# Optimization experiments

Measured on AMD Instinct MI355X. Metric: run time of the kernel, lower is better.

The kernel has to match this reference:

```python
import math
import jax, jax.numpy as jnp
import numpy as np

B, A, M, NC = 32, 8400, 32, 80
TOP_K, ALPHA, BETA, EPS = 13, 1.0, 6.0, 1e-9
IMG = 640.0


def _ciou(b1, b2, eps=1e-7):
    # b1, b2 broadcastable [..., 4]; CIoU as in compute_iou (box1=gt, box2=pred)
    b1x1, b1y1, b1x2, b1y2 = b1[..., 0], b1[..., 1], b1[..., 2], b1[..., 3]
    b2x1, b2y1, b2x2, b2y2 = b2[..., 0], b2[..., 1], b2[..., 2], b2[..., 3]
    w1, h1 = b1x2 - b1x1, b1y2 - b1y1 + eps
    w2, h2 = b2x2 - b2x1, b2y2 - b2y1 + eps
    inter = (jnp.minimum(b1x2, b2x2) - jnp.maximum(b1x1, b2x1)).clip(0) * \
            (jnp.minimum(b1y2, b2y2) - jnp.maximum(b1y1, b2y1)).clip(0)
    union = w1 * h1 + w2 * h2 - inter + eps
    iou = inter / union
    cw = jnp.maximum(b1x2, b2x2) - jnp.minimum(b1x1, b2x1)
    ch = jnp.maximum(b1y2, b2y2) - jnp.minimum(b1y1, b2y1)
    c2 = cw ** 2 + ch ** 2 + eps
    rho2 = ((b2x1 + b2x2 - b1x1 - b1x2) ** 2 + (b2y1 + b2y2 - b1y1 - b1y2) ** 2) / 4.0
    v = (4.0 / math.pi ** 2) * (jnp.arctan(w2 / h2) - jnp.arctan(w1 / h1)) ** 2
    alpha = jax.lax.stop_gradient(v / (v - iou + (1.0 + eps)))
    return iou - (rho2 / c2 + v * alpha)


def setup_inputs() -> dict:
    key = jax.random.key(0)
    ks = jax.random.split(key, 8)
    pd_scores = jax.random.uniform(ks[0], (B, A, NC), jnp.float32)
    anc_points = jax.random.uniform(ks[1], (A, 2), jnp.float32) * IMG
    # predicted boxes around anchor points (valid x1<x2, y1<y2)
    off = jax.random.uniform(ks[2], (B, A, 4), jnp.float32) * 80.0 + 2.0
    pd_bboxes = jnp.concatenate([anc_points[None] - off[..., :2],
                                 anc_points[None] + off[..., 2:]], -1)
    # GT boxes: random centers and sizes, clipped to image
    c = jax.random.uniform(ks[3], (B, M, 2), jnp.float32) * IMG
    wh = jax.random.uniform(ks[4], (B, M, 2), jnp.float32) * 180.0 + 20.0
    gt_bboxes = jnp.concatenate([(c - wh / 2).clip(0, IMG), (c + wh / 2).clip(0, IMG)], -1)
    gt_labels = jax.random.randint(ks[5], (B, M, 1), 0, NC, jnp.int64)
    n_valid = jax.random.randint(ks[6], (B,), 1, M + 1)
    mask_gt = (jnp.arange(M)[None, :] < n_valid[:, None]).astype(jnp.float32)[..., None]
    return {"pd_scores": pd_scores, "pd_bboxes": pd_bboxes, "anc_points": anc_points,
            "gt_labels": gt_labels, "gt_bboxes": gt_bboxes, "mask_gt": mask_gt}


def reference(pd_scores, pd_bboxes, anc_points, gt_labels, gt_bboxes, mask_gt):
    b, a, nc = pd_scores.shape
    m = gt_bboxes.shape[1]
    dtype = pd_scores.dtype

    # anchors-inside-GT mask: [B,M,A]
    lt = gt_bboxes[:, :, None, :2]          # [B,M,1,2]
    rb = gt_bboxes[:, :, None, 2:]
    deltas = jnp.concatenate([anc_points[None, None] - lt,
                              rb - anc_points[None, None]], -1)  # [B,M,A,4]
    mask_in_gts = deltas.min(-1) > EPS
    mg = mask_gt[..., 0] > 0                 # [B,M] bool
    gt_mask = mask_in_gts & mg[:, :, None]

    # per-GT class score gather: pd_scores[b, :, gt_labels[b,m]] -> [B,M,A]
    labels = gt_labels[..., 0]               # [B,M]
    idx = jnp.broadcast_to(labels[:, :, None, None], (b, m, a, 1))
    gathered = jnp.take_along_axis(jnp.broadcast_to(pd_scores[:, None], (b, m, a, nc)), idx, axis=3)[..., 0]
    bbox_scores = jnp.where(gt_mask, gathered, 0.0)

    # CIoU overlaps (dense, masked) [B,M,A]
    iou = _ciou(gt_bboxes[:, :, None, :], pd_bboxes[:, None, :, :])
    overlaps = jnp.where(gt_mask, jnp.maximum(iou, 0.0), 0.0)

    align_metric = bbox_scores ** ALPHA * overlaps ** BETA

    # top-k selection with duplicate suppression (faithful to scatter_add loop)
    _, tk_idx = jax.lax.top_k(align_metric, TOP_K)      # [B,M,K]
    tk_mask = jnp.broadcast_to(mg[:, :, None], tk_idx.shape)
    tk_idx = jnp.where(tk_mask, tk_idx, 0)
    bi = jnp.arange(b)[:, None, None]
    mi = jnp.arange(m)[None, :, None]
    counts = jnp.zeros((b, m, a), jnp.int32).at[bi, mi, tk_idx].add(1)
    mask_top_k = jnp.where(counts > 1, 0, counts).astype(dtype)

    mask_pos = mask_top_k * mask_in_gts.astype(dtype) * mg[:, :, None].astype(dtype)
    fg_mask = mask_pos.sum(1)                            # [B,A]

    # resolve anchors assigned to multiple GTs (no-op when none; matches torch branch)
    mask_multi = fg_mask[:, None, :] > 1                 # [B,M,A] (broadcast)
    max_idx = overlaps.argmax(1)                         # [B,A]
    is_max = (jnp.arange(m)[None, :, None] == max_idx[:, None, :]).astype(dtype)
    mask_pos = jnp.where(mask_multi, is_max, mask_pos)
    fg_mask = mask_pos.sum(1)

    target_gt_idx = mask_pos.argmax(1)                   # [B,A]
    target_labels = jnp.maximum(jnp.take_along_axis(labels, target_gt_idx, axis=1), 0)
    target_bboxes = jnp.take_along_axis(
        gt_bboxes, jnp.broadcast_to(target_gt_idx[..., None], (b, a, 4)), axis=1)

    target_scores = jax.nn.one_hot(target_labels, NC, dtype=dtype)
    target_scores = jnp.where((fg_mask > 0)[..., None], target_scores, 0.0)

    am = align_metric * mask_pos
    pos_am = am.max(-1, keepdims=True)                   # [B,M,1]
    pos_ov = (overlaps * mask_pos).max(-1, keepdims=True)
    norm = (am * pos_ov / (pos_am + EPS)).max(1)[..., None]  # [B,A,1]
    target_scores = target_scores * norm

    return target_bboxes, target_scores, fg_mask > 0
```

## Files before the change

kernel.cpp:

```cpp
#include <hip/hip_runtime.h>
#include <math.h>

#define BB 32
#define AA 8400
#define MM 32
#define NCC 80
#define TOPK 13
#define CAP 1024

__device__ __forceinline__ void wave_argmax(float& v, int& i) {
    #pragma unroll
    for (int off = 32; off > 0; off >>= 1) {
        float ov = __shfl_xor(v, off, 64);
        int oi = __shfl_xor(i, off, 64);
        if (ov > v || (ov == v && oi < i)) { v = ov; i = oi; }
    }
}

__global__ __launch_bounds__(256) void k12_topk(
        const float* __restrict__ pd_scores, const float* __restrict__ pd_bboxes,
        const float* __restrict__ anc, const int* __restrict__ gt_labels,
        const float* __restrict__ gt_bboxes, const float* __restrict__ mask_gt,
        unsigned char* __restrict__ mpos, float* __restrict__ pos_am, float* __restrict__ pos_ov) {
    __shared__ float lval[CAP];
    __shared__ int   lidx[CAP];
    __shared__ unsigned int bmask[(AA + 31) / 32];
    __shared__ float wv[4];
    __shared__ int   wi[4];
    __shared__ int   cnt, pcnt;
    const float eps = 1e-7f;
    int bm = blockIdx.x;
    int b = bm >> 5;
    int tid = threadIdx.x;
    long row = (long)bm * AA;
    if (tid == 0) { pos_am[bm] = 0.f; pos_ov[bm] = 0.f; cnt = 0; pcnt = 0; }
    unsigned int* mp4 = reinterpret_cast<unsigned int*>(mpos + row);
    for (int i = tid; i < AA / 4; i += 256) mp4[i] = 0u;
    if (!(mask_gt[bm] > 0.f)) return;

    for (int i = tid; i < (AA + 31) / 32; i += 256) bmask[i] = 0u;
    float4 g = reinterpret_cast<const float4*>(gt_bboxes)[bm];
    __syncthreads();

    #pragma unroll
    for (int j = 0; j < 33; j++) {
        int i = tid + (j << 8);
        if (i < AA) {
            float2 an = reinterpret_cast<const float2*>(anc)[i];
            float dmin = fminf(fminf(an.x - g.x, an.y - g.y), fminf(g.z - an.x, g.w - an.y));
            if (dmin > 1e-9f) {
                int s = atomicAdd(&cnt, 1);
                if (s < CAP) lidx[s] = i;
            }
        }
    }
    __syncthreads();
    int n_c = min(cnt, CAP);

    float w1 = g.z - g.x, h1 = g.w - g.y + eps;
    float atg = atanf(w1 / h1);
    float w1h1 = w1 * h1;
    float sgx = g.x + g.z, sgy = g.y + g.w;
    int lab = gt_labels[bm];
    const float4* pbb = reinterpret_cast<const float4*>(pd_bboxes) + (long)b * AA;
    const float* scp = pd_scores + (long)b * AA * NCC + lab;
    for (int s = tid; s < n_c; s += 256) {
        int i = lidx[s];
        float4 pb = pbb[i];
        float w2 = pb.z - pb.x, h2 = pb.w - pb.y + eps;
        float iw = fmaxf(fminf(g.z, pb.z) - fmaxf(g.x, pb.x), 0.f);
        float ih = fmaxf(fminf(g.w, pb.w) - fmaxf(g.y, pb.y), 0.f);
        float inter = iw * ih;
        float uni = w1h1 + w2 * h2 - inter + eps;
        float iou = inter / uni;
        float cw = fmaxf(g.z, pb.z) - fminf(g.x, pb.x);
        float ch = fmaxf(g.w, pb.w) - fminf(g.y, pb.y);
        float c2 = cw * cw + ch * ch + eps;
        float dx = pb.x + pb.z - sgx, dy = pb.y + pb.w - sgy;
        float rho2 = (dx * dx + dy * dy) * 0.25f;
        float dv = atanf(w2 / h2) - atg;
        float v = 0.4052847345693511f * dv * dv;
        float alpha = v / (v - iou + (1.0f + eps));
        float cv = iou - (rho2 / c2 + v * alpha);
        float ov = fmaxf(cv, 0.f);
        float sc = scp[(long)i * NCC];
        float o2 = ov * ov;
        float val = sc * o2 * o2 * o2;
        if (val > 0.f) {
            lval[s] = val;
            atomicAdd(&pcnt, 1);
            atomicOr(&bmask[i >> 5], 1u << (i & 31));
        } else {
            lval[s] = -1.f;
        }
    }
    for (int s = n_c + tid; s < CAP; s += 256) { lval[s] = -1.f; lidx[s] = AA; }
    __syncthreads();
    int p = pcnt;

    if (p >= TOPK) {
        float v0 = lval[tid], v1 = lval[tid + 256], v2 = lval[tid + 512], v3 = lval[tid + 768];
        int   i0 = lidx[tid], i1 = lidx[tid + 256], i2 = lidx[tid + 512], i3 = lidx[tid + 768];
        for (int k = 0; k < TOPK; k++) {
            float bv = v0; int bi = i0;
            if (v1 > bv || (v1 == bv && i1 < bi)) { bv = v1; bi = i1; }
            if (v2 > bv || (v2 == bv && i2 < bi)) { bv = v2; bi = i2; }
            if (v3 > bv || (v3 == bv && i3 < bi)) { bv = v3; bi = i3; }
            wave_argmax(bv, bi);
            if ((tid & 63) == 0) { wv[tid >> 6] = bv; wi[tid >> 6] = bi; }
            __syncthreads();
            float gv = wv[0]; int gi = wi[0];
            #pragma unroll
            for (int w = 1; w < 4; w++) {
                float ov = wv[w]; int oi = wi[w];
                if (ov > gv || (ov == gv && oi < gi)) { gv = ov; gi = oi; }
            }
            if (tid == 0) mpos[row + gi] = 1;
            if (i0 == gi) v0 = -1.f;
            if (i1 == gi) v1 = -1.f;
            if (i2 == gi) v2 = -1.f;
            if (i3 == gi) v3 = -1.f;
            __syncthreads();
        }
    } else {
        for (int s = tid; s < n_c; s += 256)
            if (lval[s] > 0.f) mpos[row + lidx[s]] = 1;
        if (tid == 0) {
            int rem = TOPK - p;
            for (int i = 0; rem > 0 && i < AA; i++) {
                if (!((bmask[i >> 5] >> (i & 31)) & 1u)) {
                    rem--;
                    float ax = anc[i * 2], ay = anc[i * 2 + 1];
                    float dmin = fminf(fminf(ax - g.x, ay - g.y), fminf(g.z - ax, g.w - ay));
                    if (dmin > 1e-9f) mpos[row + i] = 1;
                }
            }
        }
    }
}

__global__ __launch_bounds__(256) void k3_resolve(
        const float* __restrict__ pd_scores, const float* __restrict__ pd_bboxes,
        const float* __restrict__ anc, const int* __restrict__ gt_labels,
        const float* __restrict__ gt_bboxes, const float* __restrict__ mask_gt,
        const unsigned char* __restrict__ mpos,
        float* __restrict__ pos_am, float* __restrict__ pos_ov,
        float* __restrict__ out_bbox, float* __restrict__ out_fg,
        float* __restrict__ amval, int* __restrict__ packed) {
    __shared__ float sg[MM][8];
    __shared__ int slab[MM];
    __shared__ int smg[MM];
    const float eps = 1e-7f;
    int b = blockIdx.y;
    int tid = threadIdx.x;
    if (tid < MM) {
        int gm = b * MM + tid;
        float4 g = reinterpret_cast<const float4*>(gt_bboxes)[gm];
        float w1 = g.z - g.x, h1 = g.w - g.y + eps;
        sg[tid][0] = g.x; sg[tid][1] = g.y; sg[tid][2] = g.z; sg[tid][3] = g.w;
        sg[tid][4] = w1 * h1;
        sg[tid][5] = atanf(w1 / h1);
        sg[tid][6] = g.x + g.z;
        sg[tid][7] = g.y + g.w;
        int lb = gt_labels[gm]; if (lb < 0) lb = 0;
        slab[tid] = lb;
        smg[tid] = mask_gt[gm] > 0.f ? 1 : 0;
    }
    __syncthreads();
    int a = blockIdx.x * 256 + tid;
    if (a >= AA) return;
    float ax = anc[a * 2], ay = anc[a * 2 + 1];
    float4 pb = reinterpret_cast<const float4*>(pd_bboxes)[b * AA + a];
    float w2 = pb.z - pb.x, h2 = pb.w - pb.y + eps;
    float atp = atanf(w2 / h2);
    float w2h2 = w2 * h2;
    float spx = pb.x + pb.z, spy = pb.y + pb.w;
    long mbase = (long)b * MM * AA + a;

    int fg = 0, firstm = -1, bestm = 0;
    float bestov = -1.f, ovsel = 0.f;
    for (int m = 0; m < MM; m++) {
        float gx1 = sg[m][0], gy1 = sg[m][1], gx2 = sg[m][2], gy2 = sg[m][3];
        float dmin = fminf(fminf(ax - gx1, ay - gy1), fminf(gx2 - ax, gy2 - ay));
        float ov = 0.f;
        if ((dmin > 1e-9f) && smg[m]) {
            float iw = fmaxf(fminf(gx2, pb.z) - fmaxf(gx1, pb.x), 0.f);
            float ih = fmaxf(fminf(gy2, pb.w) - fmaxf(gy1, pb.y), 0.f);
            float inter = iw * ih;
            float uni = sg[m][4] + w2h2 - inter + eps;
            float iou = inter / uni;
            float cw = fmaxf(gx2, pb.z) - fminf(gx1, pb.x);
            float ch = fmaxf(gy2, pb.w) - fminf(gy1, pb.y);
            float c2 = cw * cw + ch * ch + eps;
            float dx = spx - sg[m][6], dy = spy - sg[m][7];
            float rho2 = (dx * dx + dy * dy) * 0.25f;
            float dv = atp - sg[m][5];
            float v = 0.4052847345693511f * dv * dv;
            float alpha = v / (v - iou + (1.0f + eps));
            float cv = iou - (rho2 / c2 + v * alpha);
            ov = fmaxf(cv, 0.f);
        }
        if (ov > bestov) { bestov = ov; bestm = m; }
        if (mpos[mbase + (long)m * AA]) {
            if (fg == 0) { firstm = m; ovsel = ov; }
            fg++;
        }
    }
    int tg; bool fgo; float ovt;
    if (fg > 1) { tg = bestm; fgo = true;  ovt = bestov; }
    else        { tg = (fg == 1) ? firstm : 0; fgo = (fg == 1); ovt = (fg == 1) ? ovsel : 0.f; }

    int g = b * AA + a;
    float4 gb; gb.x = sg[tg][0]; gb.y = sg[tg][1]; gb.z = sg[tg][2]; gb.w = sg[tg][3];
    reinterpret_cast<float4*>(out_bbox)[g] = gb;
    out_fg[g] = fgo ? 1.f : 0.f;
    float amv = 0.f;
    if (fgo) {
        float sc = pd_scores[((long)b * AA + a) * NCC + slab[tg]];
        float o2 = ovt * ovt;
        amv = sc * o2 * o2 * o2;
        atomicMax((int*)&pos_am[b * MM + tg], __float_as_int(amv));
        atomicMax((int*)&pos_ov[b * MM + tg], __float_as_int(ovt));
    }
    amval[g] = amv;
    packed[g] = tg | (slab[tg] << 8) | ((fgo ? 1 : 0) << 16);
}

__global__ __launch_bounds__(256) void k4_scores(
        const float* __restrict__ amval, const int* __restrict__ packed,
        const float* __restrict__ pos_am, const float* __restrict__ pos_ov,
        float* __restrict__ out_scores) {
    int g = blockIdx.x * 256 + threadIdx.x;
    const int NQ = NCC / 4;
    if (g >= BB * AA * NQ) return;
    int ba = g / NQ;
    int c0 = (g % NQ) * 4;
    float4 o = {0.f, 0.f, 0.f, 0.f};
    int p = packed[ba];
    if (p & (1 << 16)) {
        int tg = p & 31, lab = (p >> 8) & 127;
        int b = ba / AA;
        int bm = b * MM + tg;
        float nv = (amval[ba] * pos_ov[bm]) / (pos_am[bm] + 1e-9f);
        int d = lab - c0;
        if (d == 0) o.x = nv; else if (d == 1) o.y = nv;
        else if (d == 2) o.z = nv; else if (d == 3) o.w = nv;
    }
    reinterpret_cast<float4*>(out_scores)[g] = o;
}

extern "C" void kernel_launch(void* const* d_in, const int* in_sizes, int n_in,
                              void* d_out, int out_size, void* d_ws, size_t ws_size,
                              hipStream_t stream) {
    const float* pd_scores = (const float*)d_in[0];
    const float* pd_bboxes = (const float*)d_in[1];
    const float* anc       = (const float*)d_in[2];
    const int*   gt_labels = (const int*)d_in[3];
    const float* gt_bboxes = (const float*)d_in[4];
    const float* mask_gt   = (const float*)d_in[5];

    const long nBMA = (long)BB * MM * AA;
    const long nBA  = (long)BB * AA;

    char* ws = (char*)d_ws;
    unsigned char* mpos = (unsigned char*)ws;  ws += nBMA;
    float* pos_am = (float*)ws;                ws += BB * MM * 4;
    float* pos_ov = (float*)ws;                ws += BB * MM * 4;
    float* amval  = (float*)ws;                ws += nBA * 4;
    int*   packed = (int*)ws;                  ws += nBA * 4;

    float* out_bbox   = (float*)d_out;
    float* out_scores = out_bbox + nBA * 4;
    float* out_fg     = out_scores + nBA * NCC;

    k12_topk<<<BB * MM, 256, 0, stream>>>(pd_scores, pd_bboxes, anc, gt_labels,
                                          gt_bboxes, mask_gt, mpos, pos_am, pos_ov);
    dim3 g3((AA + 255) / 256, BB);
    k3_resolve<<<g3, 256, 0, stream>>>(pd_scores, pd_bboxes, anc, gt_labels,
                                       gt_bboxes, mask_gt, mpos, pos_am, pos_ov,
                                       out_bbox, out_fg, amval, packed);
    long nS4 = nBA * (NCC / 4);
    k4_scores<<<(int)((nS4 + 255) / 256), 256, 0, stream>>>(amval, packed, pos_am, pos_ov, out_scores);
}
```

Measured before the change: 215.2 us.

## Replace byte mask_pos matrix with per-anchor GT bitmask and skip non-fg CIoU

The per-(b,m,a) byte array mpos (~8.6MB written and re-read) becomes a 32-bit per-anchor bitmask that the top-k kernel sets with atomicOr, and a small zero kernel clears it. The resolve kernel reads one word per anchor. It computes CIoU only for foreground anchors, and loops over all GTs only when several are selected. Shared-memory atomic counters are also aggregated per wave with ballot/popcount. This cuts global traffic and redundant CIoU work, at the cost of an extra kernel launch and global atomics.

```diff
diff --git a/kernel.cpp b/kernel.cpp
--- a/kernel.cpp
+++ b/kernel.cpp
@@ -17,11 +17,16 @@
     }
 }
 
+__global__ __launch_bounds__(256) void k0_zero(unsigned int* __restrict__ selmask) {
+    int g = blockIdx.x * 256 + threadIdx.x;
+    if (g < BB * AA / 4) reinterpret_cast<uint4*>(selmask)[g] = uint4{0u, 0u, 0u, 0u};
+}
+
 __global__ __launch_bounds__(256) void k12_topk(
         const float* __restrict__ pd_scores, const float* __restrict__ pd_bboxes,
         const float* __restrict__ anc, const int* __restrict__ gt_labels,
         const float* __restrict__ gt_bboxes, const float* __restrict__ mask_gt,
-        unsigned char* __restrict__ mpos, float* __restrict__ pos_am, float* __restrict__ pos_ov) {
+        unsigned int* __restrict__ selmask, float* __restrict__ pos_am, float* __restrict__ pos_ov) {
     __shared__ float lval[CAP];
     __shared__ int   lidx[CAP];
     __shared__ unsigned int bmask[(AA + 31) / 32];
@@ -31,11 +36,11 @@
     const float eps = 1e-7f;
     int bm = blockIdx.x;
     int b = bm >> 5;
+    int m = bm & 31;
+    unsigned int mbit = 1u << m;
     int tid = threadIdx.x;
-    long row = (long)bm * AA;
+    int lane = tid & 63;
     if (tid == 0) { pos_am[bm] = 0.f; pos_ov[bm] = 0.f; cnt = 0; pcnt = 0; }
-    unsigned int* mp4 = reinterpret_cast<unsigned int*>(mpos + row);
-    for (int i = tid; i < AA / 4; i += 256) mp4[i] = 0u;
     if (!(mask_gt[bm] > 0.f)) return;
 
     for (int i = tid; i < (AA + 31) / 32; i += 256) bmask[i] = 0u;
@@ -45,13 +50,19 @@
     #pragma unroll
     for (int j = 0; j < 33; j++) {
         int i = tid + (j << 8);
+        bool pred = false;
         if (i < AA) {
             float2 an = reinterpret_cast<const float2*>(anc)[i];
             float dmin = fminf(fminf(an.x - g.x, an.y - g.y), fminf(g.z - an.x, g.w - an.y));
-            if (dmin > 1e-9f) {
-                int s = atomicAdd(&cnt, 1);
-                if (s < CAP) lidx[s] = i;
-            }
+            pred = dmin > 1e-9f;
+        }
+        unsigned long long wm = __ballot(pred);
+        int base = 0;
+        if (lane == 0) base = atomicAdd(&cnt, __popcll(wm));
+        base = __shfl(base, 0, 64);
+        if (pred) {
+            int s = base + __popcll(wm & ((1ull << lane) - 1ull));
+            if (s < CAP) lidx[s] = i;
         }
     }
     __syncthreads();
@@ -64,35 +75,39 @@
     int lab = gt_labels[bm];
     const float4* pbb = reinterpret_cast<const float4*>(pd_bboxes) + (long)b * AA;
     const float* scp = pd_scores + (long)b * AA * NCC + lab;
-    for (int s = tid; s < n_c; s += 256) {
-        int i = lidx[s];
-        float4 pb = pbb[i];
-        float w2 = pb.z - pb.x, h2 = pb.w - pb.y + eps;
-        float iw = fmaxf(fminf(g.z, pb.z) - fmaxf(g.x, pb.x), 0.f);
-        float ih = fmaxf(fminf(g.w, pb.w) - fmaxf(g.y, pb.y), 0.f);
-        float inter = iw * ih;
-        float uni = w1h1 + w2 * h2 - inter + eps;
-        float iou = inter / uni;
-        float cw = fmaxf(g.z, pb.z) - fminf(g.x, pb.x);
-        float ch = fmaxf(g.w, pb.w) - fminf(g.y, pb.y);
-        float c2 = cw * cw + ch * ch + eps;
-        float dx = pb.x + pb.z - sgx, dy = pb.y + pb.w - sgy;
-        float rho2 = (dx * dx + dy * dy) * 0.25f;
-        float dv = atanf(w2 / h2) - atg;
-        float v = 0.4052847345693511f * dv * dv;
-        float alpha = v / (v - iou + (1.0f + eps));
-        float cv = iou - (rho2 / c2 + v * alpha);
-        float ov = fmaxf(cv, 0.f);
-        float sc = scp[(long)i * NCC];
-        float o2 = ov * ov;
-        float val = sc * o2 * o2 * o2;
-        if (val > 0.f) {
-            lval[s] = val;
-            atomicAdd(&pcnt, 1);
-            atomicOr(&bmask[i >> 5], 1u << (i & 31));
-        } else {
-            lval[s] = -1.f;
-        }
+    int nit = (n_c + 255) >> 8;
+    for (int it = 0; it < nit; it++) {
+        int s = (it << 8) + tid;
+        bool in = s < n_c;
+        bool pos = false;
+        if (in) {
+            int i = lidx[s];
+            float4 pb = pbb[i];
+            float w2 = pb.z - pb.x, h2 = pb.w - pb.y + eps;
+            float iw = fmaxf(fminf(g.z, pb.z) - fmaxf(g.x, pb.x), 0.f);
+            float ih = fmaxf(fminf(g.w, pb.w) - fmaxf(g.y, pb.y), 0.f);
+            float inter = iw * ih;
+            float uni = w1h1 + w2 * h2 - inter + eps;
+            float iou = inter / uni;
+            float cw = fmaxf(g.z, pb.z) - fminf(g.x, pb.x);
+            float ch = fmaxf(g.w, pb.w) - fminf(g.y, pb.y);
+            float c2 = cw * cw + ch * ch + eps;
+            float dx = pb.x + pb.z - sgx, dy = pb.y + pb.w - sgy;
+            float rho2 = (dx * dx + dy * dy) * 0.25f;
+            float dv = atanf(w2 / h2) - atg;
+            float v = 0.4052847345693511f * dv * dv;
+            float alpha = v / (v - iou + (1.0f + eps));
+            float cv = iou - (rho2 / c2 + v * alpha);
+            float ov = fmaxf(cv, 0.f);
+            float sc = scp[(long)i * NCC];
+            float o2 = ov * ov;
+            float val = sc * o2 * o2 * o2;
+            pos = val > 0.f;
+            lval[s] = pos ? val : -1.f;
+            if (pos) atomicOr(&bmask[i >> 5], 1u << (i & 31));
+        }
+        unsigned long long pm = __ballot(pos);
+        if (lane == 0) atomicAdd(&pcnt, __popcll(pm));
     }
     for (int s = n_c + tid; s < CAP; s += 256) { lval[s] = -1.f; lidx[s] = AA; }
     __syncthreads();
@@ -107,7 +122,7 @@
             if (v2 > bv || (v2 == bv && i2 < bi)) { bv = v2; bi = i2; }
             if (v3 > bv || (v3 == bv && i3 < bi)) { bv = v3; bi = i3; }
             wave_argmax(bv, bi);
-            if ((tid & 63) == 0) { wv[tid >> 6] = bv; wi[tid >> 6] = bi; }
+            if (lane == 0) { wv[tid >> 6] = bv; wi[tid >> 6] = bi; }
             __syncthreads();
             float gv = wv[0]; int gi = wi[0];
             #pragma unroll
@@ -115,7 +130,7 @@
                 float ov = wv[w]; int oi = wi[w];
                 if (ov > gv || (ov == gv && oi < gi)) { gv = ov; gi = oi; }
             }
-            if (tid == 0) mpos[row + gi] = 1;
+            if (tid == 0) atomicOr(&selmask[b * AA + gi], mbit);
             if (i0 == gi) v0 = -1.f;
             if (i1 == gi) v1 = -1.f;
             if (i2 == gi) v2 = -1.f;
@@ -124,7 +139,7 @@
         }
     } else {
         for (int s = tid; s < n_c; s += 256)
-            if (lval[s] > 0.f) mpos[row + lidx[s]] = 1;
+            if (lval[s] > 0.f) atomicOr(&selmask[b * AA + lidx[s]], mbit);
         if (tid == 0) {
             int rem = TOPK - p;
             for (int i = 0; rem > 0 && i < AA; i++) {
@@ -132,7 +147,7 @@
                     rem--;
                     float ax = anc[i * 2], ay = anc[i * 2 + 1];
                     float dmin = fminf(fminf(ax - g.x, ay - g.y), fminf(g.z - ax, g.w - ay));
-                    if (dmin > 1e-9f) mpos[row + i] = 1;
+                    if (dmin > 1e-9f) atomicOr(&selmask[b * AA + i], mbit);
                 }
             }
         }
@@ -143,7 +158,7 @@
         const float* __restrict__ pd_scores, const float* __restrict__ pd_bboxes,
         const float* __restrict__ anc, const int* __restrict__ gt_labels,
         const float* __restrict__ gt_bboxes, const float* __restrict__ mask_gt,
-        const unsigned char* __restrict__ mpos,
+        const unsigned int* __restrict__ selmask,
         float* __restrict__ pos_am, float* __restrict__ pos_ov,
         float* __restrict__ out_bbox, float* __restrict__ out_fg,
         float* __restrict__ amval, int* __restrict__ packed) {
@@ -169,54 +184,70 @@
     __syncthreads();
     int a = blockIdx.x * 256 + tid;
     if (a >= AA) return;
-    float ax = anc[a * 2], ay = anc[a * 2 + 1];
-    float4 pb = reinterpret_cast<const float4*>(pd_bboxes)[b * AA + a];
-    float w2 = pb.z - pb.x, h2 = pb.w - pb.y + eps;
-    float atp = atanf(w2 / h2);
-    float w2h2 = w2 * h2;
-    float spx = pb.x + pb.z, spy = pb.y + pb.w;
-    long mbase = (long)b * MM * AA + a;
-
-    int fg = 0, firstm = -1, bestm = 0;
-    float bestov = -1.f, ovsel = 0.f;
-    for (int m = 0; m < MM; m++) {
-        float gx1 = sg[m][0], gy1 = sg[m][1], gx2 = sg[m][2], gy2 = sg[m][3];
-        float dmin = fminf(fminf(ax - gx1, ay - gy1), fminf(gx2 - ax, gy2 - ay));
-        float ov = 0.f;
-        if ((dmin > 1e-9f) && smg[m]) {
+    int g = b * AA + a;
+    unsigned int sel = selmask[g];
+    int fg = __popc(sel);
+
+    int tg = 0; bool fgo = false; float ovt = 0.f;
+    if (fg >= 1) {
+        float ax = anc[a * 2], ay = anc[a * 2 + 1];
+        float4 pb = reinterpret_cast<const float4*>(pd_bboxes)[g];
+        float w2 = pb.z - pb.x, h2 = pb.w - pb.y + eps;
+        float atp = atanf(w2 / h2);
+        float w2h2 = w2 * h2;
+        float spx = pb.x + pb.z, spy = pb.y + pb.w;
+        fgo = true;
+        if (fg == 1) {
+            tg = __ffs(sel) - 1;
+            float gx1 = sg[tg][0], gy1 = sg[tg][1], gx2 = sg[tg][2], gy2 = sg[tg][3];
             float iw = fmaxf(fminf(gx2, pb.z) - fmaxf(gx1, pb.x), 0.f);
             float ih = fmaxf(fminf(gy2, pb.w) - fmaxf(gy1, pb.y), 0.f);
             float inter = iw * ih;
-            float uni = sg[m][4] + w2h2 - inter + eps;
+            float uni = sg[tg][4] + w2h2 - inter + eps;
             float iou = inter / uni;
             float cw = fmaxf(gx2, pb.z) - fminf(gx1, pb.x);
             float ch = fmaxf(gy2, pb.w) - fminf(gy1, pb.y);
             float c2 = cw * cw + ch * ch + eps;
-            float dx = spx - sg[m][6], dy = spy - sg[m][7];
+            float dx = spx - sg[tg][6], dy = spy - sg[tg][7];
             float rho2 = (dx * dx + dy * dy) * 0.25f;
-            float dv = atp - sg[m][5];
+            float dv = atp - sg[tg][5];
             float v = 0.4052847345693511f * dv * dv;
             float alpha = v / (v - iou + (1.0f + eps));
-            float cv = iou - (rho2 / c2 + v * alpha);
-            ov = fmaxf(cv, 0.f);
-        }
-        if (ov > bestov) { bestov = ov; bestm = m; }
-        if (mpos[mbase + (long)m * AA]) {
-            if (fg == 0) { firstm = m; ovsel = ov; }
-            fg++;
-        }
-    }
-    int tg; bool fgo; float ovt;
-    if (fg > 1) { tg = bestm; fgo = true;  ovt = bestov; }
-    else        { tg = (fg == 1) ? firstm : 0; fgo = (fg == 1); ovt = (fg == 1) ? ovsel : 0.f; }
-
-    int g = b * AA + a;
+            ovt = fmaxf(iou - (rho2 / c2 + v * alpha), 0.f);
+        } else {
+            float bestov = -1.f; int bestm = 0;
+            for (int mm = 0; mm < MM; mm++) {
+                float gx1 = sg[mm][0], gy1 = sg[mm][1], gx2 = sg[mm][2], gy2 = sg[mm][3];
+                float dmin = fminf(fminf(ax - gx1, ay - gy1), fminf(gx2 - ax, gy2 - ay));
+                float ov = 0.f;
+                if ((dmin > 1e-9f) && smg[mm]) {
+                    float iw = fmaxf(fminf(gx2, pb.z) - fmaxf(gx1, pb.x), 0.f);
+                    float ih = fmaxf(fminf(gy2, pb.w) - fmaxf(gy1, pb.y), 0.f);
+                    float inter = iw * ih;
+                    float uni = sg[mm][4] + w2h2 - inter + eps;
+                    float iou = inter / uni;
+                    float cw = fmaxf(gx2, pb.z) - fminf(gx1, pb.x);
+                    float ch = fmaxf(gy2, pb.w) - fminf(gy1, pb.y);
+                    float c2 = cw * cw + ch * ch + eps;
+                    float dx = spx - sg[mm][6], dy = spy - sg[mm][7];
+                    float rho2 = (dx * dx + dy * dy) * 0.25f;
+                    float dv = atp - sg[mm][5];
+                    float v = 0.4052847345693511f * dv * dv;
+                    float alpha = v / (v - iou + (1.0f + eps));
+                    ov = fmaxf(iou - (rho2 / c2 + v * alpha), 0.f);
+                }
+                if (ov > bestov) { bestov = ov; bestm = mm; }
+            }
+            tg = bestm; ovt = bestov;
+        }
+    }
+
     float4 gb; gb.x = sg[tg][0]; gb.y = sg[tg][1]; gb.z = sg[tg][2]; gb.w = sg[tg][3];
     reinterpret_cast<float4*>(out_bbox)[g] = gb;
     out_fg[g] = fgo ? 1.f : 0.f;
     float amv = 0.f;
     if (fgo) {
-        float sc = pd_scores[((long)b * AA + a) * NCC + slab[tg]];
+        float sc = pd_scores[(long)g * NCC + slab[tg]];
         float o2 = ovt * ovt;
         amv = sc * o2 * o2 * o2;
         atomicMax((int*)&pos_am[b * MM + tg], __float_as_int(amv));
@@ -259,25 +290,25 @@
     const float* gt_bboxes = (const float*)d_in[4];
     const float* mask_gt   = (const float*)d_in[5];
 
-    const long nBMA = (long)BB * MM * AA;
-    const long nBA  = (long)BB * AA;
+    const long nBA = (long)BB * AA;
 
     char* ws = (char*)d_ws;
-    unsigned char* mpos = (unsigned char*)ws;  ws += nBMA;
-    float* pos_am = (float*)ws;                ws += BB * MM * 4;
-    float* pos_ov = (float*)ws;                ws += BB * MM * 4;
-    float* amval  = (float*)ws;                ws += nBA * 4;
-    int*   packed = (int*)ws;                  ws += nBA * 4;
+    unsigned int* selmask = (unsigned int*)ws;  ws += nBA * 4;
+    float* pos_am = (float*)ws;                 ws += BB * MM * 4;
+    float* pos_ov = (float*)ws;                 ws += BB * MM * 4;
+    float* amval  = (float*)ws;                 ws += nBA * 4;
+    int*   packed = (int*)ws;                   ws += nBA * 4;
 
     float* out_bbox   = (float*)d_out;
     float* out_scores = out_bbox + nBA * 4;
     float* out_fg     = out_scores + nBA * NCC;
 
+    k0_zero<<<(int)((nBA / 4 + 255) / 256), 256, 0, stream>>>(selmask);
     k12_topk<<<BB * MM, 256, 0, stream>>>(pd_scores, pd_bboxes, anc, gt_labels,
-                                          gt_bboxes, mask_gt, mpos, pos_am, pos_ov);
+                                          gt_bboxes, mask_gt, selmask, pos_am, pos_ov);
     dim3 g3((AA + 255) / 256, BB);
     k3_resolve<<<g3, 256, 0, stream>>>(pd_scores, pd_bboxes, anc, gt_labels,
-                                       gt_bboxes, mask_gt, mpos, pos_am, pos_ov,
+                                       gt_bboxes, mask_gt, selmask, pos_am, pos_ov,
                                        out_bbox, out_fg, amval, packed);
     long nS4 = nBA * (NCC / 4);
     k4_scores<<<(int)((nS4 + 255) / 256), 256, 0, stream>>>(amval, packed, pos_am, pos_ov, out_scores);
```

New measurement: 205.1 us. 4.7% less time.
